# Kernel tuning notes

Measured on AMD Instinct MI355X. Metric: run time of the kernel, lower is better.

The kernel has to match this reference:

```python
import jax, jax.numpy as jnp
import numpy as np

K = 8      # neighbors (from __init__ default k=8)
EPS = 1e-5 # BatchNorm1d default eps


def conv1x1(x, w, b):
    # x: (B,C,N), w: (O,C), b: (O,) -> (B,O,N)
    return jnp.einsum('bcn,oc->bon', x, w) + b[None, :, None]


def batchnorm(x, g, be):
    # training-mode BatchNorm1d: stats over (B, N) per channel
    m = x.mean(axis=(0, 2), keepdims=True)
    v = x.var(axis=(0, 2), keepdims=True)
    return g[None, :, None] * (x - m) * jax.lax.rsqrt(v + EPS) + be[None, :, None]


def block(x, w, b, g, be):
    return jax.nn.relu(batchnorm(conv1x1(x, w, b), g, be))


def setup_inputs() -> dict:
    key = jax.random.key(0)
    ks = jax.random.split(key, 24)
    B, N = 16, 4096
    rn = lambda k, s, sc=0.1: jax.random.normal(k, s, jnp.float32) * sc
    ones_n = lambda k, s: jnp.ones(s, jnp.float32) + rn(k, s, 0.01)
    return {
        'points': jax.random.normal(ks[0], (B, N, 3), jnp.float32),
        'w1': rn(ks[1], (64, 3)),   'b1': rn(ks[2], (64,)),
        'g1': ones_n(ks[3], (64,)), 'be1': rn(ks[4], (64,)),
        'w3': rn(ks[5], (512, 64)), 'b3': rn(ks[6], (512,)),
        'g3': ones_n(ks[7], (512,)), 'be3': rn(ks[8], (512,)),
        'hw1': rn(ks[9], (512, 1088)), 'hb1': rn(ks[10], (512,)),
        'hg1': ones_n(ks[11], (512,)), 'hbe1': rn(ks[12], (512,)),
        'hw2': rn(ks[13], (256, 512)), 'hb2': rn(ks[14], (256,)),
        'hg2': ones_n(ks[15], (256,)), 'hbe2': rn(ks[16], (256,)),
        'hw3': rn(ks[17], (128, 256)), 'hb3': rn(ks[18], (128,)),
        'hg3': ones_n(ks[19], (128,)), 'hbe3': rn(ks[20], (128,)),
        'hw4': rn(ks[21], (6, 128)), 'hb4': rn(ks[22], (6,)),
    }


def reference(points, w1, b1, g1, be1, w3, b3, g3, be3,
              hw1, hb1, hg1, hbe1, hw2, hb2, hg2, hbe2,
              hw3, hb3, hg3, hbe3, hw4, hb4):
    B, N, _ = points.shape
    # brute-force KNN (squared L2, ascending -> top_k on -dist)
    x2 = jnp.sum(points * points, axis=-1)                     # (B,N)
    dist = x2[:, :, None] + x2[:, None, :] \
        - 2.0 * jnp.einsum('bnd,bmd->bnm', points, points)      # (B,N,N)
    idx = jax.lax.top_k(-dist, K)[1]                           # (B,N,K) int32

    p = points.transpose(0, 2, 1)                              # (B,3,N)
    l_feat = block(p, w1, b1, g1, be1)                         # (B,64,N)
    x = block(l_feat, w3, b3, g3, be3)                         # (B,512,N)
    x_t = x.transpose(0, 2, 1)                                 # (B,N,512)

    # Faithful to the original's gather bug:
    # out[b,n,k,c] = x_t[b, idx[b,n,k], k]  (independent of c since K<512)
    vals = jnp.take_along_axis(x_t[:, :, :K], idx, axis=1)     # (B,N,K)
    m = vals.max(axis=2)                                       # (B,N)
    local_features = jnp.broadcast_to(m[:, None, :], (B, 512, N))

    global_feat = jnp.broadcast_to(x.max(axis=2, keepdims=True), (B, 512, N))
    h = jnp.concatenate([local_features, l_feat, global_feat], axis=1)  # (B,1088,N)
    h = block(h, hw1, hb1, hg1, hbe1)
    h = block(h, hw2, hb2, hg2, hbe2)
    h = block(h, hw3, hb3, hg3, hbe3)
    h = conv1x1(h, hw4, hb4)                                   # (B,6,N)
    return h.transpose(0, 2, 1)                                # (B,N,6)
```

## Files before the change

### kernel.cpp

```cpp
#include <hip/hip_runtime.h>
#include <hip/hip_bf16.h>
#include <math.h>

typedef __attribute__((ext_vector_type(8))) short short8;
typedef __attribute__((ext_vector_type(16))) float f32x16;

__device__ inline f32x16 mfma32(short8 a, short8 b, f32x16 c) {
    return __builtin_amdgcn_mfma_f32_32x32x16_bf16(a, b, c, 0, 0, 0);
}

__device__ inline void bsplit(float x, ushort& h, ushort& l) {
    __hip_bfloat16 bh = __float2bfloat16(x);
    float hf = __bfloat162float(bh);
    __hip_bfloat16 bl = __float2bfloat16(x - hf);
    h = *reinterpret_cast<ushort*>(&bh);
    l = *reinterpret_cast<ushort*>(&bl);
}

__device__ inline float unmap_f(unsigned int mp) {
    unsigned int db = mp ^ (0x80000000u | (unsigned int)((int)(~mp) >> 31));
    return __uint_as_float(db);
}

__global__ void k_wsplit_all(
    const float* __restrict__ w3s, const float* __restrict__ hw1,
    const float* __restrict__ hw2, const float* __restrict__ hw3,
    const float* __restrict__ hw4,
    ushort* __restrict__ w3h, ushort* __restrict__ w3l,
    ushort* __restrict__ w1eh, ushort* __restrict__ w1el,
    ushort* __restrict__ w2h, ushort* __restrict__ w2l,
    ushort* __restrict__ wh3h, ushort* __restrict__ wh3l,
    ushort* __restrict__ w4h, ushort* __restrict__ w4l) {
    int i = blockIdx.x * 256 + threadIdx.x;
    const float* src; int rs, co, Ms, K, base; ushort *hi, *lo;
    if (i < 32768)       { src = w3s; rs = 64;   co = 0;   Ms = 512; K = 64;  hi = w3h;  lo = w3l;  base = 0; }
    else if (i < 65536)  { src = hw1; rs = 1088; co = 512; Ms = 512; K = 64;  hi = w1eh; lo = w1el; base = 32768; }
    else if (i < 196608) { src = hw2; rs = 512;  co = 0;   Ms = 256; K = 512; hi = w2h;  lo = w2l;  base = 65536; }
    else if (i < 229376) { src = hw3; rs = 256;  co = 0;   Ms = 128; K = 256; hi = wh3h; lo = wh3l; base = 196608; }
    else if (i < 233472) { src = hw4; rs = 128;  co = 0;   Ms = 6;   K = 128; hi = w4h;  lo = w4l;  base = 229376; }
    else return;
    int li = i - base;
    int o = li / K, k = li - o * K;
    float x = (o < Ms) ? src[(size_t)o * rs + co + k] : 0.f;
    ushort h, l;
    bsplit(x, h, l);
    hi[li] = h; lo[li] = l;
}

__global__ void k_stats1(const float* __restrict__ pts, const float* __restrict__ w1,
                         const float* __restrict__ b1, float* __restrict__ part1) {
    __shared__ float sw[256];
    __shared__ float wred[2][4][64];
    int t = threadIdx.x;
    if (t < 192) sw[t] = w1[t];
    if (t < 64) sw[192 + t] = b1[t];
    __syncthreads();
    int g = blockIdx.x * 256 + t;
    float p0 = pts[g*3], p1 = pts[g*3+1], p2 = pts[g*3+2];
    int lane = t & 63, wv = t >> 6;
    for (int c = 0; c < 64; c++) {
        float y = fmaf(sw[c*3+2], p2, fmaf(sw[c*3+1], p1, fmaf(sw[c*3], p0, sw[192+c])));
        float s = y, q = y * y;
        #pragma unroll
        for (int o = 32; o > 0; o >>= 1) { s += __shfl_down(s, o); q += __shfl_down(q, o); }
        if (lane == 0) { wred[0][wv][c] = s; wred[1][wv][c] = q; }
    }
    __syncthreads();
    if (t < 64) {
        float s = wred[0][0][t] + wred[0][1][t] + wred[0][2][t] + wred[0][3][t];
        float q = wred[1][0][t] + wred[1][1][t] + wred[1][2][t] + wred[1][3][t];
        part1[blockIdx.x * 128 + t] = s;
        part1[blockIdx.x * 128 + 64 + t] = q;
    }
}

__global__ void k_fin(const float* __restrict__ part, int count, int stride, int sqoff,
                      const float* __restrict__ g, const float* __restrict__ be,
                      float* __restrict__ sout, float* __restrict__ tout) {
    int c = blockIdx.x, t = threadIdx.x;
    float s = 0.f, q = 0.f;
    for (int w = t; w < count; w += 256) { s += part[(size_t)w*stride + c]; q += part[(size_t)w*stride + sqoff + c]; }
    __shared__ float rs[4], rq[4];
    int lane = t & 63, wv = t >> 6;
    #pragma unroll
    for (int o = 32; o > 0; o >>= 1) { s += __shfl_down(s, o); q += __shfl_down(q, o); }
    if (lane == 0) { rs[wv] = s; rq[wv] = q; }
    __syncthreads();
    if (t == 0) {
        s = rs[0] + rs[1] + rs[2] + rs[3];
        q = rq[0] + rq[1] + rq[2] + rq[3];
        float mean = s / 65536.f;
        float var = q / 65536.f - mean * mean;
        float sc = g[c] * rsqrtf(var + 1e-5f);
        sout[c] = sc;
        tout[c] = be[c] - mean * sc;
    }
}

__global__ void k_lfeat2(const float* __restrict__ pts, const float* __restrict__ w1,
                         const float* __restrict__ b1, const float* __restrict__ s1,
                         const float* __restrict__ t1, ushort* __restrict__ lfh,
                         ushort* __restrict__ lfl) {
    __shared__ float sw[256], ss[64], st[64];
    int t = threadIdx.x;
    if (t < 192) sw[t] = w1[t];
    if (t < 64) { sw[192+t] = b1[t]; ss[t] = s1[t]; st[t] = t1[t]; }
    __syncthreads();
    int g = blockIdx.x * 256 + t;
    float p0 = pts[g*3], p1 = pts[g*3+1], p2 = pts[g*3+2];
    for (int c0 = 0; c0 < 64; c0 += 8) {
        union { short8 v; ushort u[8]; } H, L;
        #pragma unroll
        for (int j = 0; j < 8; j++) {
            int c = c0 + j;
            float y = fmaf(sw[c*3+2], p2, fmaf(sw[c*3+1], p1, fmaf(sw[c*3], p0, sw[192+c])));
            float a = fmaxf(fmaf(ss[c], y, st[c]), 0.f);
            bsplit(a, H.u[j], L.u[j]);
        }
        *(short8*)(lfh + (size_t)g*64 + c0) = H.v;
        *(short8*)(lfl + (size_t)g*64 + c0) = L.v;
    }
}

template<int MODE>
__global__ __launch_bounds__(256, 2) void k_gemm64(
    const ushort* __restrict__ Bhi, const ushort* __restrict__ Blo,
    const ushort* __restrict__ Ahi, const ushort* __restrict__ Alo,
    const float* __restrict__ bias, const float* __restrict__ A1,
    const float* __restrict__ G1, const float* __restrict__ mb,
    float* __restrict__ part, float* __restrict__ y38) {
    __shared__ ushort sbh[128*64], sbl[128*64];
    __shared__ float sPb[512], sPa[512];
    int t = threadIdx.x, pb = blockIdx.x;
    int gn0 = pb * 128, b = pb >> 5;
    for (int i = t; i < 512; i += 256) {
        float bb = bias[i];
        if (MODE) bb += G1[(b<<9) + i];
        sPb[i] = bb;
        sPa[i] = MODE ? A1[i] : 0.f;
    }
    for (int it = 0; it < 4; it++) {
        int s = it*256 + t;
        int n = s >> 3, c16 = s & 7;
        int off = (c16*16) ^ ((n & 7) << 4);
        int sb8 = (it*256 + (t & 192)) * 8;
        __builtin_amdgcn_global_load_lds((const char*)Bhi + (size_t)(gn0+n)*128 + off, &sbh[sb8], 16, 0, 0);
        __builtin_amdgcn_global_load_lds((const char*)Blo + (size_t)(gn0+n)*128 + off, &sbl[sb8], 16, 0, 0);
    }
    __syncthreads();
    int lane = t & 63, wv = t >> 6, m = lane & 31, kg = lane >> 5;
    for (int ct = 0; ct < 4; ct++) {
        int ch0 = wv*128 + ct*32;
        short8 ah[4], al[4];
        #pragma unroll
        for (int ks = 0; ks < 4; ks++) {
            ah[ks] = *(const short8*)(Ahi + (size_t)(ch0+m)*64 + ks*16 + kg*8);
            al[ks] = *(const short8*)(Alo + (size_t)(ch0+m)*64 + ks*16 + kg*8);
        }
        float ssum[16] = {}, ssq[16] = {}, smx[16];
        #pragma unroll
        for (int r = 0; r < 16; r++) smx[r] = -__builtin_inff();
        for (int pt = 0; pt < 4; pt++) {
            int n = pt*32 + m;
            f32x16 acc = {};
            #pragma unroll
            for (int ks = 0; ks < 4; ks++) {
                int off = ((ks*16 + kg*8)*2) ^ ((n & 7) << 4);
                short8 bh = *(const short8*)((const char*)sbh + n*128 + off);
                short8 bl = *(const short8*)((const char*)sbl + n*128 + off);
                acc = mfma32(ah[ks], bh, acc);
                acc = mfma32(ah[ks], bl, acc);
                acc = mfma32(al[ks], bh, acc);
            }
            float mval = MODE ? mb[gn0 + n] : 0.f;
            #pragma unroll
            for (int r = 0; r < 16; r++) {
                int chr = ch0 + (r&3) + 8*(r>>2) + 4*kg;
                float v = acc[r] + sPb[chr] + (MODE ? sPa[chr]*mval : 0.f);
                ssum[r] += v; ssq[r] = fmaf(v, v, ssq[r]);
                if (MODE == 0) {
                    smx[r] = fmaxf(smx[r], v);
                    if (wv == 0 && ct == 0 && r < 4) {
                        int c8 = (r&3) + 4*kg;
                        y38[(size_t)c8*65536 + gn0 + n] = v;
                    }
                }
            }
        }
        #pragma unroll
        for (int r = 0; r < 16; r++) {
            float s = ssum[r], q = ssq[r], x = smx[r];
            #pragma unroll
            for (int o = 16; o > 0; o >>= 1) {
                s += __shfl_xor(s, o); q += __shfl_xor(q, o);
                if (MODE == 0) x = fmaxf(x, __shfl_xor(x, o));
            }
            if (m == 0) {
                int chr = ch0 + (r&3) + 8*(r>>2) + 4*kg;
                if (MODE == 0) {
                    part[(size_t)pb*1536 + chr] = s;
                    part[(size_t)pb*1536 + 512 + chr] = q;
                    part[(size_t)pb*1536 + 1024 + chr] = x;
                } else {
                    part[(size_t)pb*1024 + chr] = s;
                    part[(size_t)pb*1024 + 512 + chr] = q;
                }
            }
        }
    }
}

__global__ void k_fin3b(const float* __restrict__ part3, const float* __restrict__ s3,
                        const float* __restrict__ t3, float* __restrict__ gmaxb) {
    int b = blockIdx.x, c = threadIdx.x;
    float mx = -__builtin_inff();
    for (int i = 0; i < 32; i++) mx = fmaxf(mx, part3[(size_t)(b*32+i)*1536 + 1024 + c]);
    gmaxb[(b<<9)+c] = fmaxf(fmaf(s3[c], mx, t3[c]), 0.f);
}

__global__ void k_a1g1(const float* __restrict__ hw1, const float* __restrict__ gmaxb,
                       float* __restrict__ A1, float* __restrict__ G1) {
    __shared__ float sg[512];
    int blk = blockIdx.x, t = threadIdx.x;
    if (blk < 32) {
        int b = blk >> 1;
        for (int i = t; i < 512; i += 256) sg[i] = gmaxb[(b<<9)+i];
        __syncthreads();
        int o = (blk & 1)*256 + t;
        float s = 0.f;
        for (int c4 = 0; c4 < 128; c4++) {
            float4 w = *(const float4*)&hw1[(size_t)o*1088 + 576 + c4*4];
            s = fmaf(w.x, sg[c4*4],   s);
            s = fmaf(w.y, sg[c4*4+1], s);
            s = fmaf(w.z, sg[c4*4+2], s);
            s = fmaf(w.w, sg[c4*4+3], s);
        }
        G1[(b<<9)+o] = s;
    } else {
        int o = (blk - 32)*256 + t;
        float s = 0.f;
        for (int c4 = 0; c4 < 128; c4++) {
            float4 w = *(const float4*)&hw1[(size_t)o*1088 + c4*4];
            s += w.x; s += w.y; s += w.z; s += w.w;
        }
        A1[o] = s;
    }
}

__global__ __launch_bounds__(1024, 8)
void k_knn(const float* __restrict__ pts, const float* __restrict__ y38,
           const float* __restrict__ s3, const float* __restrict__ t3,
           float* __restrict__ mbuf) {
    __shared__ float4 sp[4096];
    int t = threadIdx.x, blk = blockIdx.x;
    int b = blk >> 5;
    int lane = t & 63, wv = t >> 6;
    const float* pb = pts + (size_t)b * 4096 * 3;
    for (int i = t; i < 4096; i += 1024) {
        float c0 = pb[i*3], c1 = pb[i*3+1], c2 = pb[i*3+2];
        float cw = __fadd_rn(__fadd_rn(__fmul_rn(c0,c0), __fmul_rn(c1,c1)), __fmul_rn(c2,c2));
        sp[i] = make_float4(c0, c1, c2, cw);
    }
    __syncthreads();
    const int NINF = 0xff800000;
    int qbase = (blk & 31) * 128 + wv * 8;
    for (int pass = 0; pass < 2; ++pass) {
        int qb = qbase + pass*4;
        float q0[4], q1[4], q2[4], qx2[4];
        #pragma unroll
        for (int qi = 0; qi < 4; qi++) {
            float4 qp = sp[qb + qi];
            q0[qi] = qp.x; q1[qi] = qp.y; q2[qi] = qp.z; qx2[qi] = qp.w;
        }
        float sd[4]; unsigned int si[4]; float thr[4];
        {
            float4 cp = sp[lane];
            #pragma unroll
            for (int qi = 0; qi < 4; qi++) {
                float dot = __fadd_rn(__fadd_rn(__fmul_rn(q0[qi],cp.x), __fmul_rn(q1[qi],cp.y)), __fmul_rn(q2[qi],cp.z));
                float d = __fsub_rn(__fadd_rn(qx2[qi], cp.w), __fmul_rn(2.f, dot));
                unsigned int db = __float_as_uint(d);
                unsigned int mp = db ^ (0x80000000u | (unsigned int)((int)db >> 31));
                unsigned long long key = ((unsigned long long)mp << 32) | (unsigned int)lane;
                #pragma unroll
                for (int k = 2; k <= 64; k <<= 1) {
                    #pragma unroll
                    for (int jj = k >> 1; jj >= 1; jj >>= 1) {
                        unsigned long long pk = __shfl_xor(key, jj);
                        bool up = ((lane & k) == 0);
                        bool lower = ((lane & jj) == 0);
                        bool keepmin = (lower == up);
                        unsigned long long mn = (pk < key) ? pk : key;
                        unsigned long long mx = (pk < key) ? key : pk;
                        key = keepmin ? mn : mx;
                    }
                }
                sd[qi] = unmap_f((unsigned int)(key >> 32));
                si[qi] = (unsigned int)key;
                thr[qi] = __shfl(sd[qi], 7);
            }
        }
        for (int j = 1; j < 64; j++) {
            float4 cp = sp[j*64 + lane];
            #pragma unroll
            for (int qi = 0; qi < 4; qi++) {
                float dot = __fadd_rn(__fadd_rn(__fmul_rn(q0[qi],cp.x), __fmul_rn(q1[qi],cp.y)), __fmul_rn(q2[qi],cp.z));
                float d = __fsub_rn(__fadd_rn(qx2[qi], cp.w), __fmul_rn(2.f, dot));
                unsigned long long mask = __ballot(d < thr[qi]);
                if (mask != 0ull) {
                    do {
                        int src = __ffsll(mask) - 1;
                        float db = __uint_as_float(__builtin_amdgcn_readlane(__float_as_uint(d), src));
                        unsigned int mb_ = (unsigned int)(j*64 + src);
                        float pd = __int_as_float(__builtin_amdgcn_update_dpp(
                            NINF, __float_as_int(sd[qi]), 0x111, 0xf, 0xf, false));
                        unsigned int pi = (unsigned int)__builtin_amdgcn_update_dpp(
                            0, (int)si[qi], 0x111, 0xf, 0xf, false);
                        bool keep = (sd[qi] <= db);
                        bool pk = (pd <= db);
                        sd[qi] = keep ? sd[qi] : (pk ? db : pd);
                        si[qi] = keep ? si[qi] : (pk ? mb_ : pi);
                        mask &= (mask - 1ull);
                    } while (mask != 0ull);
                    thr[qi] = __shfl(sd[qi], 7);
                }
            }
        }
        if (lane < 8) {
            #pragma unroll
            for (int qi = 0; qi < 4; qi++) {
                float y = y38[(size_t)lane*65536 + (b<<12) + (si[qi] & 4095)];
                float mv = fmaxf(fmaf(s3[lane], y, t3[lane]), 0.f);
                mv = fmaxf(mv, __shfl_xor(mv, 1));
                mv = fmaxf(mv, __shfl_xor(mv, 2));
                mv = fmaxf(mv, __shfl_xor(mv, 4));
                if (lane == 0) mbuf[(b<<12) + qb + qi] = mv;
            }
        }
    }
}

__global__ __launch_bounds__(256, 2) void k_h2f(
    const ushort* __restrict__ lfh, const ushort* __restrict__ lfl,
    const ushort* __restrict__ W1hi, const ushort* __restrict__ W1lo,
    const ushort* __restrict__ W2hi, const ushort* __restrict__ W2lo,
    const float* __restrict__ hb1, const float* __restrict__ A1g,
    const float* __restrict__ G1g, const float* __restrict__ mb,
    const float* __restrict__ sh1, const float* __restrict__ th1,
    const float* __restrict__ hb2,
    float* __restrict__ pre2, float* __restrict__ parth2) {
    __shared__ ushort sLh[128*64], sLl[128*64];
    __shared__ ushort a1h[128*64], a1l[128*64];
    __shared__ float sP0[512], sP1[512], sSh[512];
    int t = threadIdx.x, pb = blockIdx.x;
    int gn0 = pb * 128, b = pb >> 5;
    for (int i = t; i < 512; i += 256) {
        float s = sh1[i];
        sP0[i] = fmaf(s, hb1[i] + G1g[(b<<9)+i], th1[i]);
        sP1[i] = s * A1g[i];
        sSh[i] = s;
    }
    for (int it = 0; it < 4; it++) {
        int s = it*256 + t;
        int n = s >> 3, c16 = s & 7;
        int off = (c16*16) ^ ((n & 7) << 4);
        int sb8 = (it*256 + (t & 192)) * 8;
        __builtin_amdgcn_global_load_lds((const char*)lfh + (size_t)(gn0+n)*128 + off, &sLh[sb8], 16, 0, 0);
        __builtin_amdgcn_global_load_lds((const char*)lfl + (size_t)(gn0+n)*128 + off, &sLl[sb8], 16, 0, 0);
    }
    __syncthreads();
    int lane = t & 63, wv = t >> 6, m = lane & 31, kg = lane >> 5;
    int pn = wv*32 + m;
    float mval = mb[gn0 + pn];
    f32x16 acc0[4] = {}, acc1[4] = {};
    for (int ch = 0; ch < 8; ch++) {
        #pragma unroll
        for (int cht = 0; cht < 2; cht++) {
            int cch = ch*64 + cht*32;
            f32x16 acc = {};
            #pragma unroll
            for (int ks = 0; ks < 4; ks++) {
                short8 ah = *(const short8*)(W1hi + (size_t)(cch+m)*64 + ks*16 + kg*8);
                short8 al = *(const short8*)(W1lo + (size_t)(cch+m)*64 + ks*16 + kg*8);
                int off = ((ks*16 + kg*8)*2) ^ ((m & 7) << 4);
                short8 bh = *(const short8*)((const char*)sLh + pn*128 + off);
                short8 bl = *(const short8*)((const char*)sLl + pn*128 + off);
                acc = mfma32(ah, bh, acc);
                acc = mfma32(ah, bl, acc);
                acc = mfma32(al, bh, acc);
            }
            #pragma unroll
            for (int q = 0; q < 4; q++) {
                ushort hs[4], ls[4];
                #pragma unroll
                for (int i = 0; i < 4; i++) {
                    int r = q*4 + i;
                    int chr = cch + i + 8*q + 4*kg;
                    float a = fmaxf(fmaf(sSh[chr], acc[r], sP0[chr] + sP1[chr]*mval), 0.f);
                    bsplit(a, hs[i], ls[i]);
                }
                int chb = cht*32 + 8*q + 4*kg;
                int off = (chb*2) ^ ((m & 7) << 4);
                uint2 vh, vl;
                vh.x = (uint)hs[0] | ((uint)hs[1] << 16); vh.y = (uint)hs[2] | ((uint)hs[3] << 16);
                vl.x = (uint)ls[0] | ((uint)ls[1] << 16); vl.y = (uint)ls[2] | ((uint)ls[3] << 16);
                *(uint2*)((char*)a1h + pn*128 + off) = vh;
                *(uint2*)((char*)a1l + pn*128 + off) = vl;
            }
        }
        __syncthreads();
        #pragma unroll
        for (int ks = 0; ks < 4; ks++) {
            int koc = ks*16 + kg*8;
            int kglob = ch*64 + koc;
            short8 w0h = *(const short8*)(W2hi + (size_t)(wv*64+m)*512 + kglob);
            short8 w0l = *(const short8*)(W2lo + (size_t)(wv*64+m)*512 + kglob);
            short8 w1h = *(const short8*)(W2hi + (size_t)(wv*64+32+m)*512 + kglob);
            short8 w1l = *(const short8*)(W2lo + (size_t)(wv*64+32+m)*512 + kglob);
            #pragma unroll
            for (int pt = 0; pt < 4; pt++) {
                int n = pt*32 + m;
                int off = (koc*2) ^ ((n & 7) << 4);
                short8 bh = *(const short8*)((const char*)a1h + n*128 + off);
                short8 bl = *(const short8*)((const char*)a1l + n*128 + off);
                acc0[pt] = mfma32(w0h, bh, acc0[pt]);
                acc1[pt] = mfma32(w1h, bh, acc1[pt]);
                acc0[pt] = mfma32(w0h, bl, acc0[pt]);
                acc1[pt] = mfma32(w1h, bl, acc1[pt]);
                acc0[pt] = mfma32(w0l, bh, acc0[pt]);
                acc1[pt] = mfma32(w1l, bh, acc1[pt]);
            }
        }
        __syncthreads();
    }
    #pragma unroll
    for (int ti = 0; ti < 2; ti++) {
        #pragma unroll
        for (int r = 0; r < 16; r++) {
            int chr = wv*64 + ti*32 + (r&3) + 8*(r>>2) + 4*kg;
            float hb = hb2[chr];
            float s = 0.f, q = 0.f;
            #pragma unroll
            for (int pt = 0; pt < 4; pt++) {
                float v = (ti ? acc1[pt][r] : acc0[pt][r]) + hb;
                pre2[(size_t)chr*65536 + gn0 + pt*32 + m] = v;
                s += v; q = fmaf(v, v, q);
            }
            #pragma unroll
            for (int o = 16; o > 0; o >>= 1) { s += __shfl_xor(s, o); q += __shfl_xor(q, o); }
            if (m == 0) {
                parth2[(size_t)pb*512 + chr] = s;
                parth2[(size_t)pb*512 + 256 + chr] = q;
            }
        }
    }
}

__global__ __launch_bounds__(256, 2) void k_h3s(
    const float* __restrict__ pre2, const float* __restrict__ sh2,
    const float* __restrict__ th2,
    const ushort* __restrict__ W3hi, const ushort* __restrict__ W3lo,
    const float* __restrict__ hb3, float* __restrict__ parth3) {
    __shared__ ushort sbh[32*256], sbl[32*256];
    __shared__ float ft[128*36];
    __shared__ float sS2[256], sT2[256];
    int t = threadIdx.x, pb = blockIdx.x;
    sS2[t] = sh2[t]; sT2[t] = th2[t];
    int lane = t & 63, wv = t >> 6, m = lane & 31, kg = lane >> 5;
    int ch0 = wv * 32;
    int cn = t & 31, cgq = t >> 5;
    float bhr[16];
    #pragma unroll
    for (int r = 0; r < 16; r++) bhr[r] = hb3[ch0 + (r&3) + 8*(r>>2) + 4*kg];
    float ssum[16] = {}, ssq[16] = {};
    for (int pt = 0; pt < 4; pt++) {
        int gn0 = pb*128 + pt*32;
        for (int h = 0; h < 2; h++) {
            __syncthreads();
            #pragma unroll
            for (int i = 0; i < 4; i++) {
                int idx = i*256 + t;
                int row = idx >> 3, c4 = idx & 7;
                float4 v = *(const float4*)(pre2 + (size_t)(h*128+row)*65536 + gn0 + c4*4);
                float* dst = &ft[row*36 + c4*4];
                dst[0] = v.x; dst[1] = v.y; dst[2] = v.z; dst[3] = v.w;
            }
            __syncthreads();
            #pragma unroll
            for (int i4 = 0; i4 < 4; i4++) {
                int cl0 = cgq*16 + i4*4;
                int cg0 = h*128 + cl0;
                ushort hs[4], ls[4];
                #pragma unroll
                for (int i = 0; i < 4; i++) {
                    float v = fmaxf(fmaf(sS2[cg0+i], ft[(cl0+i)*36 + cn], sT2[cg0+i]), 0.f);
                    bsplit(v, hs[i], ls[i]);
                }
                int off = cn*512 + (((cg0 >> 3)*16) ^ ((cn & 15) << 4)) + (cg0 & 7)*2;
                uint2 vh, vl;
                vh.x = (uint)hs[0] | ((uint)hs[1] << 16); vh.y = (uint)hs[2] | ((uint)hs[3] << 16);
                vl.x = (uint)ls[0] | ((uint)ls[1] << 16); vl.y = (uint)ls[2] | ((uint)ls[3] << 16);
                *(uint2*)((char*)sbh + off) = vh;
                *(uint2*)((char*)sbl + off) = vl;
            }
        }
        __syncthreads();
        f32x16 acc = {};
        for (int ks = 0; ks < 16; ks++) {
            int ko = ks*16 + kg*8;
            int off = (ko*2) ^ ((m & 15) << 4);
            short8 bh = *(const short8*)((const char*)sbh + m*512 + off);
            short8 bl = *(const short8*)((const char*)sbl + m*512 + off);
            short8 ah = *(const short8*)(W3hi + (size_t)(ch0+m)*256 + ko);
            short8 al = *(const short8*)(W3lo + (size_t)(ch0+m)*256 + ko);
            acc = mfma32(ah, bh, acc);
            acc = mfma32(ah, bl, acc);
            acc = mfma32(al, bh, acc);
        }
        #pragma unroll
        for (int r = 0; r < 16; r++) {
            float v = acc[r] + bhr[r];
            ssum[r] += v; ssq[r] = fmaf(v, v, ssq[r]);
        }
    }
    #pragma unroll
    for (int r = 0; r < 16; r++) {
        float s = ssum[r], q = ssq[r];
        #pragma unroll
        for (int o = 16; o > 0; o >>= 1) { s += __shfl_xor(s, o); q += __shfl_xor(q, o); }
        if (m == 0) {
            int chr = ch0 + (r&3) + 8*(r>>2) + 4*kg;
            parth3[(size_t)pb*256 + chr] = s;
            parth3[(size_t)pb*256 + 128 + chr] = q;
        }
    }
}

__global__ __launch_bounds__(256, 2) void k_h4m(
    const float* __restrict__ pre2, const float* __restrict__ sh2,
    const float* __restrict__ th2,
    const ushort* __restrict__ W3hi, const ushort* __restrict__ W3lo,
    const float* __restrict__ hb3, const float* __restrict__ sh3,
    const float* __restrict__ th3, const ushort* __restrict__ W4hi,
    const ushort* __restrict__ W4lo, const float* __restrict__ hb4,
    float* __restrict__ out) {
    __shared__ ushort sbh[32*256], sbl[32*256];
    __shared__ float ft[128*36];
    __shared__ float sS[128], sT[128], sB[128];
    __shared__ float sS2[256], sT2[256];
    ushort* a3h = (ushort*)ft;
    ushort* a3l = ((ushort*)ft) + 32*128;
    int t = threadIdx.x, pb = blockIdx.x;
    int gn0 = pb * 32;
    if (t < 128) { sS[t] = sh3[t]; sT[t] = th3[t]; sB[t] = hb3[t]; }
    sS2[t] = sh2[t]; sT2[t] = th2[t];
    int cn = t & 31, cgq = t >> 5;
    for (int h = 0; h < 2; h++) {
        __syncthreads();
        #pragma unroll
        for (int i = 0; i < 4; i++) {
            int idx = i*256 + t;
            int row = idx >> 3, c4 = idx & 7;
            float4 v = *(const float4*)(pre2 + (size_t)(h*128+row)*65536 + gn0 + c4*4);
            float* dst = &ft[row*36 + c4*4];
            dst[0] = v.x; dst[1] = v.y; dst[2] = v.z; dst[3] = v.w;
        }
        __syncthreads();
        #pragma unroll
        for (int i4 = 0; i4 < 4; i4++) {
            int cl0 = cgq*16 + i4*4;
            int cg0 = h*128 + cl0;
            ushort hs[4], ls[4];
            #pragma unroll
            for (int i = 0; i < 4; i++) {
                float v = fmaxf(fmaf(sS2[cg0+i], ft[(cl0+i)*36 + cn], sT2[cg0+i]), 0.f);
                bsplit(v, hs[i], ls[i]);
            }
            int off = cn*512 + (((cg0 >> 3)*16) ^ ((cn & 15) << 4)) + (cg0 & 7)*2;
            uint2 vh, vl;
            vh.x = (uint)hs[0] | ((uint)hs[1] << 16); vh.y = (uint)hs[2] | ((uint)hs[3] << 16);
            vl.x = (uint)ls[0] | ((uint)ls[1] << 16); vl.y = (uint)ls[2] | ((uint)ls[3] << 16);
            *(uint2*)((char*)sbh + off) = vh;
            *(uint2*)((char*)sbl + off) = vl;
        }
    }
    __syncthreads();
    int lane = t & 63, wv = t >> 6, m = lane & 31, kg = lane >> 5;
    int ch0 = wv * 32;
    f32x16 acc = {};
    for (int ks = 0; ks < 16; ks++) {
        int ko = ks*16 + kg*8;
        int off = (ko*2) ^ ((m & 15) << 4);
        short8 bh = *(const short8*)((const char*)sbh + m*512 + off);
        short8 bl = *(const short8*)((const char*)sbl + m*512 + off);
        short8 ah = *(const short8*)(W3hi + (size_t)(ch0+m)*256 + ko);
        short8 al = *(const short8*)(W3lo + (size_t)(ch0+m)*256 + ko);
        acc = mfma32(ah, bh, acc);
        acc = mfma32(ah, bl, acc);
        acc = mfma32(al, bh, acc);
    }
    #pragma unroll
    for (int q = 0; q < 4; q++) {
        ushort hs[4], ls[4];
        #pragma unroll
        for (int i = 0; i < 4; i++) {
            int r = q*4 + i;
            int chr = ch0 + i + 8*q + 4*kg;
            float v = fmaxf(fmaf(sS[chr], acc[r] + sB[chr], sT[chr]), 0.f);
            bsplit(v, hs[i], ls[i]);
        }
        int chb = ch0 + 8*q + 4*kg;
        int off = (chb*2) ^ ((m & 15) << 4);
        uint2 vh, vl;
        vh.x = (uint)hs[0] | ((uint)hs[1] << 16); vh.y = (uint)hs[2] | ((uint)hs[3] << 16);
        vl.x = (uint)ls[0] | ((uint)ls[1] << 16); vl.y = (uint)ls[2] | ((uint)ls[3] << 16);
        *(uint2*)((char*)a3h + m*256 + off) = vh;
        *(uint2*)((char*)a3l + m*256 + off) = vl;
    }
    __syncthreads();
    if (wv == 0) {
        f32x16 acc2 = {};
        for (int ks = 0; ks < 8; ks++) {
            int ko = ks*16 + kg*8;
            int off = (ko*2) ^ ((m & 15) << 4);
            short8 bh = *(const short8*)((const char*)a3h + m*256 + off);
            short8 bl = *(const short8*)((const char*)a3l + m*256 + off);
            short8 ah = *(const short8*)(W4hi + (size_t)m*128 + ko);
            short8 al = *(const short8*)(W4lo + (size_t)m*128 + ko);
            acc2 = mfma32(ah, bh, acc2);
            acc2 = mfma32(ah, bl, acc2);
            acc2 = mfma32(al, bh, acc2);
        }
        #pragma unroll
        for (int r = 0; r < 16; r++) {
            int mrow = (r&3) + 8*(r>>2) + 4*kg;
            if (mrow < 6) out[(size_t)(gn0+m)*6 + mrow] = acc2[r] + hb4[mrow];
        }
    }
}

extern "C" void kernel_launch(void* const* d_in, const int* in_sizes, int n_in,
                              void* d_out, int out_size, void* d_ws, size_t ws_size,
                              hipStream_t stream) {
    const float* pts  = (const float*)d_in[0];
    const float* w1   = (const float*)d_in[1];
    const float* b1   = (const float*)d_in[2];
    const float* g1   = (const float*)d_in[3];
    const float* be1  = (const float*)d_in[4];
    const float* w3   = (const float*)d_in[5];
    const float* b3   = (const float*)d_in[6];
    const float* g3   = (const float*)d_in[7];
    const float* be3  = (const float*)d_in[8];
    const float* hw1  = (const float*)d_in[9];
    const float* hb1  = (const float*)d_in[10];
    const float* hg1  = (const float*)d_in[11];
    const float* hbe1 = (const float*)d_in[12];
    const float* hw2  = (const float*)d_in[13];
    const float* hb2  = (const float*)d_in[14];
    const float* hg2  = (const float*)d_in[15];
    const float* hbe2 = (const float*)d_in[16];
    const float* hw3  = (const float*)d_in[17];
    const float* hb3  = (const float*)d_in[18];
    const float* hg3  = (const float*)d_in[19];
    const float* hbe3 = (const float*)d_in[20];
    const float* hw4  = (const float*)d_in[21];
    const float* hb4  = (const float*)d_in[22];
    (void)in_sizes; (void)n_in; (void)out_size; (void)ws_size;

    float* W = (float*)d_ws;
    size_t off = 0;
    auto alloc = [&](size_t n) { float* p = W + off; off += n; return p; };
    auto allocU = [&](size_t nshorts) { return (ushort*)alloc((nshorts + 1) / 2); };

    ushort* lfh  = allocU(65536UL*64);
    ushort* lfl  = allocU(65536UL*64);
    ushort* w3h  = allocU(512*64);  ushort* w3l  = allocU(512*64);
    ushort* w1eh = allocU(512*64);  ushort* w1el = allocU(512*64);
    ushort* w2h  = allocU(256*512); ushort* w2l  = allocU(256*512);
    ushort* wh3h = allocU(128*256); ushort* wh3l = allocU(128*256);
    ushort* w4h  = allocU(32*128);  ushort* w4l  = allocU(32*128);
    float* y38    = alloc(524288);
    float* mbuf   = alloc(65536);
    float* gmaxb  = alloc(8192);
    float* G1     = alloc(8192);
    float* A1     = alloc(512);
    float* s1 = alloc(64);  float* t1 = alloc(64);
    float* s3 = alloc(512); float* t3 = alloc(512);
    float* sh1 = alloc(512); float* th1 = alloc(512);
    float* sh2 = alloc(256); float* th2 = alloc(256);
    float* sh3 = alloc(128); float* th3 = alloc(128);
    float* part1  = alloc(32768);
    float* part3  = alloc(512*1536);
    float* parth1 = alloc(512*1024);
    float* parth2 = alloc(512*512);
    float* parth3 = alloc(512*256);
    float* pre2   = alloc(16777216);

    k_wsplit_all<<<912, 256, 0, stream>>>(w3, hw1, hw2, hw3, hw4,
                                          w3h, w3l, w1eh, w1el, w2h, w2l,
                                          wh3h, wh3l, w4h, w4l);

    k_stats1<<<256, 256, 0, stream>>>(pts, w1, b1, part1);
    k_fin<<<64, 256, 0, stream>>>(part1, 256, 128, 64, g1, be1, s1, t1);
    k_lfeat2<<<256, 256, 0, stream>>>(pts, w1, b1, s1, t1, lfh, lfl);
    k_gemm64<0><<<512, 256, 0, stream>>>(lfh, lfl, w3h, w3l, b3, nullptr, nullptr, nullptr, part3, y38);
    k_fin<<<512, 256, 0, stream>>>(part3, 512, 1536, 512, g3, be3, s3, t3);
    k_fin3b<<<16, 512, 0, stream>>>(part3, s3, t3, gmaxb);
    k_a1g1<<<34, 256, 0, stream>>>(hw1, gmaxb, A1, G1);
    k_knn<<<512, 1024, 0, stream>>>(pts, y38, s3, t3, mbuf);
    k_gemm64<1><<<512, 256, 0, stream>>>(lfh, lfl, w1eh, w1el, hb1, A1, G1, mbuf, parth1, nullptr);
    k_fin<<<512, 256, 0, stream>>>(parth1, 512, 1024, 512, hg1, hbe1, sh1, th1);
    k_h2f<<<512, 256, 0, stream>>>(lfh, lfl, w1eh, w1el, w2h, w2l, hb1, A1, G1, mbuf,
                                   sh1, th1, hb2, pre2, parth2);
    k_fin<<<256, 256, 0, stream>>>(parth2, 512, 512, 256, hg2, hbe2, sh2, th2);
    k_h3s<<<512, 256, 0, stream>>>(pre2, sh2, th2, wh3h, wh3l, hb3, parth3);
    k_fin<<<128, 256, 0, stream>>>(parth3, 512, 256, 128, hg3, hbe3, sh3, th3);
    k_h4m<<<2048, 256, 0, stream>>>(pre2, sh2, th2, wh3h, wh3l, hb3, sh3, th3, w4h, w4l, hb4, (float*)d_out);
}
```

Baseline: 445.2 us.

## Store layer-3 pre-activations and replace recompute kernel with light final conv

New measurement: 410.2 us (median of 2 runs). -7.9%, faster.

```diff
diff --git a/kernel.cpp b/kernel.cpp
--- a/kernel.cpp
+++ b/kernel.cpp
@@ -460,7 +460,8 @@
     const float* __restrict__ pre2, const float* __restrict__ sh2,
     const float* __restrict__ th2,
     const ushort* __restrict__ W3hi, const ushort* __restrict__ W3lo,
-    const float* __restrict__ hb3, float* __restrict__ parth3) {
+    const float* __restrict__ hb3, float* __restrict__ parth3,
+    float* __restrict__ pre3) {
     __shared__ ushort sbh[32*256], sbl[32*256];
     __shared__ float ft[128*36];
     __shared__ float sS2[256], sT2[256];
@@ -520,6 +521,8 @@
         #pragma unroll
         for (int r = 0; r < 16; r++) {
             float v = acc[r] + bhr[r];
+            int chr = ch0 + (r&3) + 8*(r>>2) + 4*kg;
+            pre3[(size_t)chr*65536 + gn0 + m] = v;
             ssum[r] += v; ssq[r] = fmaf(v, v, ssq[r]);
         }
     }
@@ -536,106 +539,38 @@
     }
 }
 
-__global__ __launch_bounds__(256, 2) void k_h4m(
-    const float* __restrict__ pre2, const float* __restrict__ sh2,
-    const float* __restrict__ th2,
-    const ushort* __restrict__ W3hi, const ushort* __restrict__ W3lo,
-    const float* __restrict__ hb3, const float* __restrict__ sh3,
-    const float* __restrict__ th3, const ushort* __restrict__ W4hi,
-    const ushort* __restrict__ W4lo, const float* __restrict__ hb4,
-    float* __restrict__ out) {
-    __shared__ ushort sbh[32*256], sbl[32*256];
-    __shared__ float ft[128*36];
-    __shared__ float sS[128], sT[128], sB[128];
-    __shared__ float sS2[256], sT2[256];
-    ushort* a3h = (ushort*)ft;
-    ushort* a3l = ((ushort*)ft) + 32*128;
+__global__ __launch_bounds__(256) void k_h4l(
+    const float* __restrict__ pre3, const float* __restrict__ sh3,
+    const float* __restrict__ th3, const float* __restrict__ hw4,
+    const float* __restrict__ hb4, float* __restrict__ out) {
+    __shared__ float a3[128*66];
+    __shared__ float sW[6*128];
+    __shared__ float sB[8];
     int t = threadIdx.x, pb = blockIdx.x;
-    int gn0 = pb * 32;
-    if (t < 128) { sS[t] = sh3[t]; sT[t] = th3[t]; sB[t] = hb3[t]; }
-    sS2[t] = sh2[t]; sT2[t] = th2[t];
-    int cn = t & 31, cgq = t >> 5;
-    for (int h = 0; h < 2; h++) {
-        __syncthreads();
-        #pragma unroll
-        for (int i = 0; i < 4; i++) {
-            int idx = i*256 + t;
-            int row = idx >> 3, c4 = idx & 7;
-            float4 v = *(const float4*)(pre2 + (size_t)(h*128+row)*65536 + gn0 + c4*4);
-            float* dst = &ft[row*36 + c4*4];
-            dst[0] = v.x; dst[1] = v.y; dst[2] = v.z; dst[3] = v.w;
-        }
-        __syncthreads();
-        #pragma unroll
-        for (int i4 = 0; i4 < 4; i4++) {
-            int cl0 = cgq*16 + i4*4;
-            int cg0 = h*128 + cl0;
-            ushort hs[4], ls[4];
-            #pragma unroll
-            for (int i = 0; i < 4; i++) {
-                float v = fmaxf(fmaf(sS2[cg0+i], ft[(cl0+i)*36 + cn], sT2[cg0+i]), 0.f);
-                bsplit(v, hs[i], ls[i]);
-            }
-            int off = cn*512 + (((cg0 >> 3)*16) ^ ((cn & 15) << 4)) + (cg0 & 7)*2;
-            uint2 vh, vl;
-            vh.x = (uint)hs[0] | ((uint)hs[1] << 16); vh.y = (uint)hs[2] | ((uint)hs[3] << 16);
-            vl.x = (uint)ls[0] | ((uint)ls[1] << 16); vl.y = (uint)ls[2] | ((uint)ls[3] << 16);
-            *(uint2*)((char*)sbh + off) = vh;
-            *(uint2*)((char*)sbl + off) = vl;
-        }
-    }
-    __syncthreads();
-    int lane = t & 63, wv = t >> 6, m = lane & 31, kg = lane >> 5;
-    int ch0 = wv * 32;
-    f32x16 acc = {};
-    for (int ks = 0; ks < 16; ks++) {
-        int ko = ks*16 + kg*8;
-        int off = (ko*2) ^ ((m & 15) << 4);
-        short8 bh = *(const short8*)((const char*)sbh + m*512 + off);
-        short8 bl = *(const short8*)((const char*)sbl + m*512 + off);
-        short8 ah = *(const short8*)(W3hi + (size_t)(ch0+m)*256 + ko);
-        short8 al = *(const short8*)(W3lo + (size_t)(ch0+m)*256 + ko);
-        acc = mfma32(ah, bh, acc);
-        acc = mfma32(ah, bl, acc);
-        acc = mfma32(al, bh, acc);
-    }
+    int n0 = pb * 64;
+    for (int i = t; i < 768; i += 256) sW[i] = hw4[i];
+    if (t < 6) sB[t] = hb4[t];
     #pragma unroll
-    for (int q = 0; q < 4; q++) {
-        ushort hs[4], ls[4];
-        #pragma unroll
-        for (int i = 0; i < 4; i++) {
-            int r = q*4 + i;
-            int chr = ch0 + i + 8*q + 4*kg;
-            float v = fmaxf(fmaf(sS[chr], acc[r] + sB[chr], sT[chr]), 0.f);
-            bsplit(v, hs[i], ls[i]);
-        }
-        int chb = ch0 + 8*q + 4*kg;
-        int off = (chb*2) ^ ((m & 15) << 4);
-        uint2 vh, vl;
-        vh.x = (uint)hs[0] | ((uint)hs[1] << 16); vh.y = (uint)hs[2] | ((uint)hs[3] << 16);
-        vl.x = (uint)ls[0] | ((uint)ls[1] << 16); vl.y = (uint)ls[2] | ((uint)ls[3] << 16);
-        *(uint2*)((char*)a3h + m*256 + off) = vh;
-        *(uint2*)((char*)a3l + m*256 + off) = vl;
-    }
-    __syncthreads();
-    if (wv == 0) {
-        f32x16 acc2 = {};
-        for (int ks = 0; ks < 8; ks++) {
-            int ko = ks*16 + kg*8;
-            int off = (ko*2) ^ ((m & 15) << 4);
-            short8 bh = *(const short8*)((const char*)a3h + m*256 + off);
-            short8 bl = *(const short8*)((const char*)a3l + m*256 + off);
-            short8 ah = *(const short8*)(W4hi + (size_t)m*128 + ko);
-            short8 al = *(const short8*)(W4lo + (size_t)m*128 + ko);
-            acc2 = mfma32(ah, bh, acc2);
-            acc2 = mfma32(ah, bl, acc2);
-            acc2 = mfma32(al, bh, acc2);
-        }
-        #pragma unroll
-        for (int r = 0; r < 16; r++) {
-            int mrow = (r&3) + 8*(r>>2) + 4*kg;
-            if (mrow < 6) out[(size_t)(gn0+m)*6 + mrow] = acc2[r] + hb4[mrow];
-        }
+    for (int k = 0; k < 32; k++) {
+        int i = k*256 + t;
+        int c = i >> 6, col = i & 63;
+        float v = pre3[(size_t)c*65536 + n0 + col];
+        a3[c*66 + col] = fmaxf(fmaf(sh3[c], v, th3[c]), 0.f);
+    }
+    __syncthreads();
+    int p = t & 63, grp = t >> 6;
+    if (grp < 3) {
+        float a0 = sB[grp*2], a1 = sB[grp*2+1];
+        const float* w0 = &sW[(grp*2)*128];
+        const float* w1 = &sW[(grp*2+1)*128];
+        #pragma unroll 4
+        for (int c = 0; c < 128; c++) {
+            float x = a3[c*66 + p];
+            a0 = fmaf(w0[c], x, a0);
+            a1 = fmaf(w1[c], x, a1);
+        }
+        out[(size_t)(n0+p)*6 + grp*2]     = a0;
+        out[(size_t)(n0+p)*6 + grp*2 + 1] = a1;
     }
 }
 
@@ -695,6 +630,7 @@
     float* parth2 = alloc(512*512);
     float* parth3 = alloc(512*256);
     float* pre2   = alloc(16777216);
+    float* pre3   = alloc(8388608);
 
     k_wsplit_all<<<912, 256, 0, stream>>>(w3, hw1, hw2, hw3, hw4,
                                           w3h, w3l, w1eh, w1el, w2h, w2l,
@@ -713,7 +649,7 @@
     k_h2f<<<512, 256, 0, stream>>>(lfh, lfl, w1eh, w1el, w2h, w2l, hb1, A1, G1, mbuf,
                                    sh1, th1, hb2, pre2, parth2);
     k_fin<<<256, 256, 0, stream>>>(parth2, 512, 512, 256, hg2, hbe2, sh2, th2);
-    k_h3s<<<512, 256, 0, stream>>>(pre2, sh2, th2, wh3h, wh3l, hb3, parth3);
+    k_h3s<<<512, 256, 0, stream>>>(pre2, sh2, th2, wh3h, wh3l, hb3, parth3, pre3);
     k_fin<<<128, 256, 0, stream>>>(parth3, 512, 256, 128, hg3, hbe3, sh3, th3);
-    k_h4m<<<2048, 256, 0, stream>>>(pre2, sh2, th2, wh3h, wh3l, hb3, sh3, th3, w4h, w4l, hb4, (float*)d_out);
-}
+    k_h4l<<<1024, 256, 0, stream>>>(pre3, sh3, th3, hw4, hb4, (float*)d_out);
+}
```
